# Optimization experiments

Measured on AMD Instinct MI355X. Metric: run time of the kernel, lower is better.

Reference implementation:

```python
import jax, jax.numpy as jnp
import numpy as np

N_T, N_C, N_D = 500_000, 200_000, 100_000  # target / card / device node counts
E = 1_000_000                              # edges per relation
IN, HID, OUT = 64, 64, 2


def setup_inputs() -> dict:
    key = jax.random.key(0)
    ks = jax.random.split(key, 18)
    f32 = jnp.float32
    inp = {
        "features": jax.random.normal(ks[0], (N_T, IN), f32),
        "emb_card": jax.random.normal(ks[1], (N_C, IN), f32) * 0.05,
        "emb_device": jax.random.normal(ks[2], (N_D, IN), f32) * 0.05,
        "W1": jax.random.normal(ks[3], (4, IN, HID), f32) * 0.05,
        "b1": jax.random.normal(ks[4], (4, HID), f32) * 0.05,
        "W2": jax.random.normal(ks[5], (4, HID, HID), f32) * 0.05,
        "b2": jax.random.normal(ks[6], (4, HID), f32) * 0.05,
        "W_out": jax.random.normal(ks[7], (HID, OUT), f32) * 0.05,
        "b_out": jax.random.normal(ks[8], (OUT,), f32) * 0.05,
        "src_c2t": jax.random.randint(ks[9], (E,), 0, N_C, jnp.int32),
        "dst_c2t": jax.random.randint(ks[10], (E,), 0, N_T, jnp.int32),
        "src_t2c": jax.random.randint(ks[11], (E,), 0, N_T, jnp.int32),
        "dst_t2c": jax.random.randint(ks[12], (E,), 0, N_C, jnp.int32),
        "src_d2t": jax.random.randint(ks[13], (E,), 0, N_D, jnp.int32),
        "dst_d2t": jax.random.randint(ks[14], (E,), 0, N_T, jnp.int32),
        "src_t2d": jax.random.randint(ks[15], (E,), 0, N_T, jnp.int32),
        "dst_t2d": jax.random.randint(ks[16], (E,), 0, N_D, jnp.int32),
    }
    return inp


def _mean_agg(Wh, src, dst, n_dst):
    """copy_u gather + scatter-mean: mean over incoming edges of Wh[src]."""
    msgs = Wh[src]  # [E, H] gather
    s = jax.ops.segment_sum(msgs, dst, num_segments=n_dst)
    deg = jax.ops.segment_sum(jnp.ones((src.shape[0],), Wh.dtype), dst, num_segments=n_dst)
    return s / jnp.maximum(deg, 1.0)[:, None]  # zero in-degree -> 0 (DGL default)


def _layer(x_t, x_c, x_d, W, b, edges):
    # etype order: 0 card->target, 1 target->card, 2 device->target, 3 target->device
    (sc2t, dc2t, st2c, dt2c, sd2t, dd2t, st2d, dt2d) = edges
    Wh0 = x_c @ W[0] + b[0]
    Wh1 = x_t @ W[1] + b[1]
    Wh2 = x_d @ W[2] + b[2]
    Wh3 = x_t @ W[3] + b[3]
    # cross-relation reducer = 'sum'
    h_t = _mean_agg(Wh0, sc2t, dc2t, N_T) + _mean_agg(Wh2, sd2t, dd2t, N_T)
    h_c = _mean_agg(Wh1, st2c, dt2c, N_C)
    h_d = _mean_agg(Wh3, st2d, dt2d, N_D)
    return h_t, h_c, h_d


def reference(features, emb_card, emb_device, W1, b1, W2, b2, W_out, b_out,
              src_c2t, dst_c2t, src_t2c, dst_t2c, src_d2t, dst_d2t, src_t2d, dst_t2d):
    edges = (src_c2t, dst_c2t, src_t2c, dst_t2c, src_d2t, dst_d2t, src_t2d, dst_t2d)
    h_t, h_c, h_d = _layer(features, emb_card, emb_device, W1, b1, edges)
    h_t, h_c, h_d = (jax.nn.leaky_relu(h, 0.01) for h in (h_t, h_c, h_d))
    h_t, h_c, h_d = _layer(h_t, h_c, h_d, W2, b2, edges)
    return h_t @ W_out + b_out  # [N_T, OUT] logits for target node type
```

## Files before the change

kernel.cpp:

```cpp
#include <hip/hip_runtime.h>
#include <hip/hip_bf16.h>


#define NT 500000
#define NC 200000
#define ND 100000
#define NE 1000000
#define H  64
#define CAP_T2C 32
#define CAP_T2D 48

#define PACK_SCALE 65536.0f
#define PACK_BIAS  262144
#define FIELD_MASK 0x3FFFFFFULL

#define NBK_MAX 245
#define OFF_C2T 196
#define OFF_D2T 441
#define EPB 4096
#define BPR 245
#define CAP_BK1 11776
#define CAP_BK2 4864

#define CB512 7813

__device__ __forceinline__ void rel_params(int rel, int& shift, int& hoff, int& nbk) {
    shift = (rel == 1) ? 10 : 11;
    hoff = (rel == 0) ? 0 : (rel == 1) ? 98 : (rel == 2) ? OFF_C2T : OFF_D2T;
    nbk = (rel < 2) ? 98 : 245;
}

__global__ __launch_bounds__(512)
void scatter_compress(const int* __restrict__ st2c, const int* __restrict__ dt2c,
                      const int* __restrict__ st2d, const int* __restrict__ dt2d,
                      const int* __restrict__ sc2t, const int* __restrict__ dc2t,
                      const int* __restrict__ sd2t, const int* __restrict__ dd2t,
                      int* __restrict__ cur,
                      unsigned long long* __restrict__ bedges1,
                      unsigned long long* __restrict__ bedges2,
                      const float* __restrict__ X, unsigned int* __restrict__ Xb,
                      const float* __restrict__ W2, const float* __restrict__ b2,
                      const float* __restrict__ Wout,
                      float* __restrict__ Wc, float* __restrict__ bc) {
    __shared__ unsigned long long le[EPB];
    __shared__ int h[NBK_MAX], pref[NBK_MAX], gbase[NBK_MAX], csr[NBK_MAX];
    __shared__ int sc[256];
    int t = threadIdx.x, b = blockIdx.x;

    if (b >= 4 * BPR) {
        int cb = b - 4 * BPR;
        if (cb < CB512) {
            size_t idx = (size_t)cb * 512 + t;
            if (idx < 4000000) {
                const float4 f0 = ((const float4*)X)[idx * 2];
                const float4 f1 = ((const float4*)X)[idx * 2 + 1];
                uint4 o;
                unsigned int u;
                #define BF(x) (u = __float_as_uint(x), (u + 0x7fffu + ((u >> 16) & 1u)) >> 16)
                o.x = BF(f0.x) | (BF(f0.y) << 16);
                o.y = BF(f0.z) | (BF(f0.w) << 16);
                o.z = BF(f1.x) | (BF(f1.y) << 16);
                o.w = BF(f1.z) | (BF(f1.w) << 16);
                #undef BF
                ((uint4*)Xb)[idx] = o;
            }
        } else if (t < 256) {
            int rel = t >> 7;
            int rem = t & 127;
            int k = rem >> 1, o = rem & 1;
            const float* W2r = W2 + (rel ? 2 : 0) * H * H;
            float s = 0.0f;
            for (int j = 0; j < H; ++j) s += W2r[k * H + j] * Wout[j * 2 + o];
            Wc[rel * 128 + k * 2 + o] = s;
            if (rem < 4) {
                int r2 = rem >> 1, o2 = rem & 1;
                const float* b2r = b2 + (r2 ? 2 : 0) * H;
                float sb = 0.0f;
                for (int j = 0; j < H; ++j) sb += b2r[j] * Wout[j * 2 + o2];
                bc[r2 * 2 + o2] = sb;
            }
        }
        return;
    }

    int rel = b / BPR;
    int bb = b - rel * BPR;
    const int* sp = (rel == 0) ? st2c : (rel == 1) ? st2d : (rel == 2) ? sc2t : sd2t;
    const int* dp = (rel == 0) ? dt2c : (rel == 1) ? dt2d : (rel == 2) ? dc2t : dd2t;
    int shift, hoff, nbk;
    rel_params(rel, shift, hoff, nbk);
    unsigned long long* bedges = (rel < 2) ? bedges1 : bedges2;
    int bkoff = (rel == 1) ? 98 : (rel == 3) ? 245 : 0;
    int bkcap = (rel < 2) ? CAP_BK1 : CAP_BK2;

    for (int i = t; i < nbk; i += 512) { h[i] = 0; csr[i] = 0; }
    __syncthreads();

    int base = bb * EPB + t * 8;
    bool ok = base < NE;
    int4 d0, d1, s0, s1;
    if (ok) {
        d0 = *(const int4*)(dp + base);
        d1 = *(const int4*)(dp + base + 4);
        s0 = *(const int4*)(sp + base);
        s1 = *(const int4*)(sp + base + 4);
        atomicAdd(&h[d0.x >> shift], 1);
        atomicAdd(&h[d0.y >> shift], 1);
        atomicAdd(&h[d0.z >> shift], 1);
        atomicAdd(&h[d0.w >> shift], 1);
        atomicAdd(&h[d1.x >> shift], 1);
        atomicAdd(&h[d1.y >> shift], 1);
        atomicAdd(&h[d1.z >> shift], 1);
        atomicAdd(&h[d1.w >> shift], 1);
    }
    __syncthreads();
    if (t < nbk && h[t]) gbase[t] = (bkoff + t) * bkcap + atomicAdd(&cur[hoff + t], h[t]);
    if (t < 256) sc[t] = (t < nbk) ? h[t] : 0;
    __syncthreads();
    for (int s = 1; s < 256; s <<= 1) {
        int y = (t < 256 && t >= s) ? sc[t - s] : 0;
        __syncthreads();
        if (t < 256) sc[t] += y;
        __syncthreads();
    }
    if (t < nbk) pref[t] = sc[t] - h[t];
    __syncthreads();

    if (ok) {
        #define BIN(dv, sv) { int k = (dv) >> shift; \
            int l = atomicAdd(&csr[k], 1); \
            le[pref[k] + l] = ((unsigned long long)(unsigned int)(dv) << 32) | (unsigned int)(sv); }
        BIN(d0.x, s0.x) BIN(d0.y, s0.y) BIN(d0.z, s0.z) BIN(d0.w, s0.w)
        BIN(d1.x, s1.x) BIN(d1.y, s1.y) BIN(d1.z, s1.z) BIN(d1.w, s1.w)
        #undef BIN
    }
    __syncthreads();

    int n_e = NE - bb * EPB; if (n_e > EPB) n_e = EPB;
    for (int i = t; i < n_e; i += 512) {
        unsigned long long e = le[i];
        int k = (int)(e >> 32) >> shift;
        bedges[(size_t)gbase[k] + (i - pref[k])] = e;
    }
}

__global__ __launch_bounds__(1024)
void radix_build(const unsigned long long* __restrict__ bedges1, const int* __restrict__ cur,
                 int* __restrict__ cnt_t2c, int* __restrict__ cols_t2c,
                 int* __restrict__ cnt_t2d, int* __restrict__ cols_t2d) {
    __shared__ int lc[2048];
    int t = threadIdx.x, k = blockIdx.x;
    int rel = k >= 98 ? 1 : 0;
    int shift = rel ? 10 : 11;
    int range = 1 << shift;
    int noff = (rel ? (k - 98) : k) << shift;
    int nN = rel ? ND : NC;
    int* cnt = rel ? cnt_t2d : cnt_t2c;
    int* cols = rel ? cols_t2d : cols_t2c;
    int cap = rel ? CAP_T2D : CAP_T2C;
    int e0 = k * CAP_BK1;
    int e1 = e0 + cur[k];
    for (int i = t; i < range; i += 1024) lc[i] = 0;
    __syncthreads();
    for (int i = e0 + t; i < e1; i += 1024) {
        unsigned long long e = bedges1[i];
        int d = (int)(e >> 32);
        int s = (int)(e & 0xffffffffu);
        int l = atomicAdd(&lc[d - noff], 1);
        if (l < cap) cols[(size_t)d * cap + l] = s;
    }
    __syncthreads();
    for (int i = t; i < range; i += 1024) {
        int gn = noff + i;
        if (gn < nN) cnt[gn] = lc[i];
    }
}

#define NBGM_C 3125
#define NBGM_D 1563

__global__ __launch_bounds__(512)
void gx_fused(const unsigned int* __restrict__ Xb,
              const int* __restrict__ cnt_c, const int* __restrict__ cols_c,
              const int* __restrict__ cnt_d, const int* __restrict__ cols_d,
              const float* __restrict__ W1, const float* __restrict__ b1,
              const float* __restrict__ Wc, const float* __restrict__ bc,
              float* __restrict__ Pc, float* __restrict__ Pd) {
    __shared__ float Xs[64][65];
    __shared__ float Wl[64][68];
    __shared__ float msk[64];
    int t = threadIdx.x;
    int lane = t & 63;
    int w = t >> 6;
    int half = lane >> 5;
    int li = lane & 31;

    int bn, nNodes, cap;
    const int* cnt; const int* cols;
    const float* W1r; const float* b1r; const float* Wcr; const float* bcr;
    float* P;
    if (blockIdx.x < NBGM_C) {
        bn = blockIdx.x * 64; nNodes = NC; cap = CAP_T2C;
        cnt = cnt_c; cols = cols_c;
        W1r = W1 + 1 * H * H; b1r = b1 + 1 * H; Wcr = Wc; bcr = bc; P = Pc;
    } else {
        bn = (blockIdx.x - NBGM_C) * 64; nNodes = ND; cap = CAP_T2D;
        cnt = cnt_d; cols = cols_d;
        W1r = W1 + 3 * H * H; b1r = b1 + 3 * H; Wcr = Wc + 128; bcr = bc + 2; P = Pd;
    }

    for (int q = t; q < 1024; q += 512) {
        int kk = q >> 4, s2 = q & 15;
        *(float4*)&Wl[kk][s2 * 4] = *(const float4*)(W1r + kk * H + s2 * 4);
    }

    int gnb = bn + w * 8;
    int cval = 0;
    if (lane < 8 && gnb + lane < nNodes) cval = cnt[gnb + lane];

    int cc[8], mm[8], cv[8];
#pragma unroll
    for (int r = 0; r < 8; ++r) {
        cc[r] = __shfl(cval, r);
        mm[r] = cc[r] < cap ? cc[r] : cap;
    }
#pragma unroll
    for (int r = 0; r < 8; ++r) {
        int gn = gnb + r;
        cv[r] = (lane < mm[r] && gn < nNodes) ? cols[(size_t)gn * cap + lane] : 0;
    }

    int maxm = 0;
#pragma unroll
    for (int r = 0; r < 8; ++r) maxm = maxm > mm[r] ? maxm : mm[r];

    float ax[8], ay[8];
#pragma unroll
    for (int r = 0; r < 8; ++r) { ax[r] = 0.0f; ay[r] = 0.0f; }

    for (int j = 0; j < maxm; j += 2) {
#pragma unroll
        for (int r = 0; r < 8; ++r) {
            int sA = __shfl(cv[r], j);
            int sB = __shfl(cv[r], j + 1);
            int src = half ? sB : sA;
            unsigned int v = 0;
            if (j + half < mm[r]) v = Xb[(size_t)src * 32 + li];
            ax[r] += __uint_as_float(v << 16);
            ay[r] += __uint_as_float(v & 0xffff0000u);
        }
    }

#pragma unroll
    for (int r = 0; r < 8; ++r) {
        float fx = ax[r] + __shfl_xor(ax[r], 32);
        float fy = ay[r] + __shfl_xor(ay[r], 32);
        float inv = cc[r] > 0 ? 1.0f / (float)cc[r] : 0.0f;
        ax[r] = fx * inv; ay[r] = fy * inv;
    }
#pragma unroll
    for (int r = 0; r < 8; r += 2) {
        int nl = w * 8 + r + half;
        float2 v = half ? make_float2(ax[r + 1], ay[r + 1]) : make_float2(ax[r], ay[r]);
        *(float2*)&Xs[nl][li * 2] = v;
    }
    if (lane < 8) msk[w * 8 + lane] = (cval > 0) ? 1.0f : 0.0f;
    __syncthreads();

    int nl = t >> 3;
    int c0 = (t & 7) * 8;
    float4 ba = *(const float4*)(b1r + c0);
    float4 bb4 = *(const float4*)(b1r + c0 + 4);
    float h0 = ba.x, h1 = ba.y, h2 = ba.z, h3 = ba.w;
    float h4 = bb4.x, h5 = bb4.y, h6 = bb4.z, h7 = bb4.w;
#pragma unroll
    for (int k = 0; k < H; ++k) {
        float xv = Xs[nl][k];
        float4 wa = *(const float4*)&Wl[k][c0];
        float4 wb = *(const float4*)&Wl[k][c0 + 4];
        h0 = fmaf(xv, wa.x, h0); h1 = fmaf(xv, wa.y, h1);
        h2 = fmaf(xv, wa.z, h2); h3 = fmaf(xv, wa.w, h3);
        h4 = fmaf(xv, wb.x, h4); h5 = fmaf(xv, wb.y, h5);
        h6 = fmaf(xv, wb.z, h6); h7 = fmaf(xv, wb.w, h7);
    }
    float m = msk[nl];
    h0 = (h0 > 0.f ? h0 : 0.01f * h0) * m;
    h1 = (h1 > 0.f ? h1 : 0.01f * h1) * m;
    h2 = (h2 > 0.f ? h2 : 0.01f * h2) * m;
    h3 = (h3 > 0.f ? h3 : 0.01f * h3) * m;
    h4 = (h4 > 0.f ? h4 : 0.01f * h4) * m;
    h5 = (h5 > 0.f ? h5 : 0.01f * h5) * m;
    h6 = (h6 > 0.f ? h6 : 0.01f * h6) * m;
    h7 = (h7 > 0.f ? h7 : 0.01f * h7) * m;
    float4 wc0 = *(const float4*)(Wcr + c0 * 2);
    float4 wc1 = *(const float4*)(Wcr + c0 * 2 + 4);
    float4 wc2 = *(const float4*)(Wcr + c0 * 2 + 8);
    float4 wc3 = *(const float4*)(Wcr + c0 * 2 + 12);
    float p0 = h0 * wc0.x + h1 * wc0.z + h2 * wc1.x + h3 * wc1.z
             + h4 * wc2.x + h5 * wc2.z + h6 * wc3.x + h7 * wc3.z;
    float p1 = h0 * wc0.y + h1 * wc0.w + h2 * wc1.y + h3 * wc1.w
             + h4 * wc2.y + h5 * wc2.w + h6 * wc3.y + h7 * wc3.w;
#pragma unroll
    for (int off = 1; off < 8; off <<= 1) {
        p0 += __shfl_xor(p0, off);
        p1 += __shfl_xor(p1, off);
    }
    int gn = bn + nl;
    if ((t & 7) == 0 && gn < nNodes) {
        float2 o = make_float2(p0 + bcr[0], p1 + bcr[1]);
        *(float2*)(P + 2 * (size_t)gn) = o;
    }
}

__device__ __forceinline__ unsigned long long pack_p(const float* __restrict__ P, int s) {
    float2 pv = *(const float2*)(P + 2 * (size_t)s);
    float a = fminf(fmaxf(pv.x, -3.99f), 3.99f);
    float b = fminf(fmaxf(pv.y, -3.99f), 3.99f);
    unsigned int ia = (unsigned int)(__float2int_rn(a * PACK_SCALE) + PACK_BIAS);
    unsigned int ib = (unsigned int)(__float2int_rn(b * PACK_SCALE) + PACK_BIAS);
    return (1ULL << 52) | ((unsigned long long)ia << 26) | (unsigned long long)ib;
}

__global__ __launch_bounds__(1024)
void agg_out(const unsigned long long* __restrict__ bedges2, const int* __restrict__ cur,
             const float* __restrict__ Pc, const float* __restrict__ Pd,
             const float* __restrict__ bout, float* __restrict__ out) {
    __shared__ unsigned long long accC[2048], accD[2048];
    int t = threadIdx.x, k = blockIdx.x;
    int noff = k << 11;
    int range = NT - noff; if (range > 2048) range = 2048;
    for (int i = t; i < 2048; i += 1024) { accC[i] = 0ULL; accD[i] = 0ULL; }
    __syncthreads();

    int e0 = k * CAP_BK2, e1 = e0 + cur[OFF_C2T + k];
    for (int i = e0 + t; i < e1; i += 1024) {
        unsigned long long e = bedges2[i];
        int d = (int)(e >> 32);
        int s = (int)(e & 0xffffffffu);
        atomicAdd(&accC[d - noff], pack_p(Pc, s));
    }
    int f0 = (245 + k) * CAP_BK2, f1 = f0 + cur[OFF_D2T + k];
    for (int i = f0 + t; i < f1; i += 1024) {
        unsigned long long e = bedges2[i];
        int d = (int)(e >> 32);
        int s = (int)(e & 0xffffffffu);
        atomicAdd(&accD[d - noff], pack_p(Pd, s));
    }
    __syncthreads();

    float bo0 = bout[0], bo1 = bout[1];
    const float inv_s = 1.0f / PACK_SCALE;
    for (int i = t; i < range; i += 1024) {
        unsigned long long xc = accC[i];
        unsigned long long xd = accD[i];
        int dc = (int)(xc >> 52);
        int dd = (int)(xd >> 52);
        float ic = dc > 0 ? 1.0f / (float)dc : 0.0f;
        float id = dd > 0 ? 1.0f / (float)dd : 0.0f;
        float c0 = (float)((long long)((xc >> 26) & FIELD_MASK) - (long long)dc * PACK_BIAS);
        float c1 = (float)((long long)(xc & FIELD_MASK) - (long long)dc * PACK_BIAS);
        float d0 = (float)((long long)((xd >> 26) & FIELD_MASK) - (long long)dd * PACK_BIAS);
        float d1 = (float)((long long)(xd & FIELD_MASK) - (long long)dd * PACK_BIAS);
        float2 o;
        o.x = bo0 + (c0 * ic + d0 * id) * inv_s;
        o.y = bo1 + (c1 * ic + d1 * id) * inv_s;
        *(float2*)(out + 2 * (size_t)(noff + i)) = o;
    }
}

extern "C" void kernel_launch(void* const* d_in, const int* in_sizes, int n_in,
                              void* d_out, int out_size, void* d_ws, size_t ws_size,
                              hipStream_t stream) {
    const float* features = (const float*)d_in[0];
    const float* W1 = (const float*)d_in[3];
    const float* b1 = (const float*)d_in[4];
    const float* W2 = (const float*)d_in[5];
    const float* b2 = (const float*)d_in[6];
    const float* W_out = (const float*)d_in[7];
    const float* b_out = (const float*)d_in[8];
    const int* src_c2t = (const int*)d_in[9];
    const int* dst_c2t = (const int*)d_in[10];
    const int* src_t2c = (const int*)d_in[11];
    const int* dst_t2c = (const int*)d_in[12];
    const int* src_d2t = (const int*)d_in[13];
    const int* dst_d2t = (const int*)d_in[14];
    const int* src_t2d = (const int*)d_in[15];
    const int* dst_t2d = (const int*)d_in[16];
    float* out = (float*)d_out;

    char* w = (char*)d_ws;
    int* cur = (int*)w;                           w += 1024 * 4;
    size_t zero_bytes = 1024 * 4;
    int* cnt_t2c = (int*)w;                       w += (size_t)NC * 4;
    int* cnt_t2d = (int*)w;                       w += (size_t)ND * 4;
    int* cols_t2c = (int*)w;                      w += (size_t)NC * CAP_T2C * 4;
    int* cols_t2d = (int*)w;                      w += (size_t)ND * CAP_T2D * 4;
    float* p_c = (float*)w;                       w += (size_t)NC * 2 * 4;
    float* p_d = (float*)w;                       w += (size_t)ND * 2 * 4;
    float* Wc = (float*)w;                        w += 256 * 4;
    float* bc = (float*)w;                        w += 16;
    unsigned long long* bedges1 = (unsigned long long*)w;  w += (size_t)196 * CAP_BK1 * 8;
    unsigned long long* bedges2 = (unsigned long long*)w;  w += (size_t)490 * CAP_BK2 * 8;
    unsigned int* Xb = (unsigned int*)w;          w += (size_t)NT * H * 2;

    hipMemsetAsync(d_ws, 0, zero_bytes, stream);

    scatter_compress<<<4 * BPR + CB512 + 1, 512, 0, stream>>>(
        src_t2c, dst_t2c, src_t2d, dst_t2d,
        src_c2t, dst_c2t, src_d2t, dst_d2t,
        cur, bedges1, bedges2,
        features, Xb, W2, b2, W_out, Wc, bc);

    radix_build<<<196, 1024, 0, stream>>>(bedges1, cur,
                                          cnt_t2c, cols_t2c, cnt_t2d, cols_t2d);

    gx_fused<<<NBGM_C + NBGM_D, 512, 0, stream>>>(
        Xb, cnt_t2c, cols_t2c, cnt_t2d, cols_t2d,
        W1, b1, Wc, bc, p_c, p_d);

    agg_out<<<NBK_MAX, 1024, 0, stream>>>(bedges2, cur, p_c, p_d, b_out, out);
}
```

Measured before the change: 210.4 us.

## Split fused gather-mean and 64x64 transform into two kernels via bf16 buffer

Splits the fused gather-plus-matmul kernel in two. The first kernel does the neighbor mean gather and writes bf16-packed means to a new workspace buffer. The second loads those rows into shared memory and does the W1/Wc projection. This frees the gather kernel from the large shared-memory tiles and the W1 load, which may raise occupancy and latency hiding for the irregular gathers. In exchange it adds a launch, an extra global round trip of about 38 MB, and one more bf16 rounding of the mean.

```diff
diff --git a/kernel.cpp b/kernel.cpp
--- a/kernel.cpp
+++ b/kernel.cpp
@@ -29,6 +29,8 @@
     hoff = (rel == 0) ? 0 : (rel == 1) ? 98 : (rel == 2) ? OFF_C2T : OFF_D2T;
     nbk = (rel < 2) ? 98 : 245;
 }
+
+#define BFP(x) (u = __float_as_uint(x), (u + 0x7fffu + ((u >> 16) & 1u)) >> 16)
 
 __global__ __launch_bounds__(512)
 void scatter_compress(const int* __restrict__ st2c, const int* __restrict__ dt2c,
@@ -56,12 +58,10 @@
                 const float4 f1 = ((const float4*)X)[idx * 2 + 1];
                 uint4 o;
                 unsigned int u;
-                #define BF(x) (u = __float_as_uint(x), (u + 0x7fffu + ((u >> 16) & 1u)) >> 16)
-                o.x = BF(f0.x) | (BF(f0.y) << 16);
-                o.y = BF(f0.z) | (BF(f0.w) << 16);
-                o.z = BF(f1.x) | (BF(f1.y) << 16);
-                o.w = BF(f1.z) | (BF(f1.w) << 16);
-                #undef BF
+                o.x = BFP(f0.x) | (BFP(f0.y) << 16);
+                o.y = BFP(f0.z) | (BFP(f0.w) << 16);
+                o.z = BFP(f1.x) | (BFP(f1.y) << 16);
+                o.w = BFP(f1.z) | (BFP(f1.w) << 16);
                 ((uint4*)Xb)[idx] = o;
             }
         } else if (t < 256) {
@@ -180,15 +180,10 @@
 #define NBGM_D 1563
 
 __global__ __launch_bounds__(512)
-void gx_fused(const unsigned int* __restrict__ Xb,
-              const int* __restrict__ cnt_c, const int* __restrict__ cols_c,
-              const int* __restrict__ cnt_d, const int* __restrict__ cols_d,
-              const float* __restrict__ W1, const float* __restrict__ b1,
-              const float* __restrict__ Wc, const float* __restrict__ bc,
-              float* __restrict__ Pc, float* __restrict__ Pd) {
-    __shared__ float Xs[64][65];
-    __shared__ float Wl[64][68];
-    __shared__ float msk[64];
+void gather_mean(const unsigned int* __restrict__ Xb,
+                 const int* __restrict__ cnt_c, const int* __restrict__ cols_c,
+                 const int* __restrict__ cnt_d, const int* __restrict__ cols_d,
+                 unsigned int* __restrict__ mB) {
     int t = threadIdx.x;
     int lane = t & 63;
     int w = t >> 6;
@@ -196,22 +191,13 @@
     int li = lane & 31;
 
     int bn, nNodes, cap;
-    const int* cnt; const int* cols;
-    const float* W1r; const float* b1r; const float* Wcr; const float* bcr;
-    float* P;
+    const int* cnt; const int* cols; unsigned int* mP;
     if (blockIdx.x < NBGM_C) {
         bn = blockIdx.x * 64; nNodes = NC; cap = CAP_T2C;
-        cnt = cnt_c; cols = cols_c;
-        W1r = W1 + 1 * H * H; b1r = b1 + 1 * H; Wcr = Wc; bcr = bc; P = Pc;
+        cnt = cnt_c; cols = cols_c; mP = mB;
     } else {
         bn = (blockIdx.x - NBGM_C) * 64; nNodes = ND; cap = CAP_T2D;
-        cnt = cnt_d; cols = cols_d;
-        W1r = W1 + 3 * H * H; b1r = b1 + 3 * H; Wcr = Wc + 128; bcr = bc + 2; P = Pd;
-    }
-
-    for (int q = t; q < 1024; q += 512) {
-        int kk = q >> 4, s2 = q & 15;
-        *(float4*)&Wl[kk][s2 * 4] = *(const float4*)(W1r + kk * H + s2 * 4);
+        cnt = cnt_d; cols = cols_d; mP = mB + (size_t)NC * 32;
     }
 
     int gnb = bn + w * 8;
@@ -258,13 +244,60 @@
         float inv = cc[r] > 0 ? 1.0f / (float)cc[r] : 0.0f;
         ax[r] = fx * inv; ay[r] = fy * inv;
     }
+    unsigned int u;
 #pragma unroll
     for (int r = 0; r < 8; r += 2) {
-        int nl = w * 8 + r + half;
-        float2 v = half ? make_float2(ax[r + 1], ay[r + 1]) : make_float2(ax[r], ay[r]);
-        *(float2*)&Xs[nl][li * 2] = v;
-    }
-    if (lane < 8) msk[w * 8 + lane] = (cval > 0) ? 1.0f : 0.0f;
+        int gn = gnb + r + half;
+        float vx = half ? ax[r + 1] : ax[r];
+        float vy = half ? ay[r + 1] : ay[r];
+        unsigned int pv = BFP(vx) | (BFP(vy) << 16);
+        if (gn < nNodes) mP[(size_t)gn * 32 + li] = pv;
+    }
+}
+
+#define NBX_C 3125
+#define NBX_D 1563
+
+__global__ __launch_bounds__(512)
+void xform64(const unsigned int* __restrict__ mB,
+             const int* __restrict__ cnt_c, const int* __restrict__ cnt_d,
+             const float* __restrict__ W1, const float* __restrict__ b1,
+             const float* __restrict__ Wc, const float* __restrict__ bc,
+             float* __restrict__ Pc, float* __restrict__ Pd) {
+    __shared__ float Xs[64][65];
+    __shared__ float Wl[64][68];
+    __shared__ float msk[64];
+    int t = threadIdx.x;
+
+    int bn, nNodes; const unsigned int* mrow; const int* cnt;
+    const float* W1r; const float* b1r; const float* Wcr; const float* bcr;
+    float* P;
+    if (blockIdx.x < NBX_C) {
+        bn = blockIdx.x * 64; nNodes = NC;
+        mrow = mB; cnt = cnt_c;
+        W1r = W1 + 1 * H * H; b1r = b1 + 1 * H; Wcr = Wc; bcr = bc; P = Pc;
+    } else {
+        bn = (blockIdx.x - NBX_C) * 64; nNodes = ND;
+        mrow = mB + (size_t)NC * 32; cnt = cnt_d;
+        W1r = W1 + 3 * H * H; b1r = b1 + 3 * H; Wcr = Wc + 128; bcr = bc + 2; P = Pd;
+    }
+
+    {
+        int nl = t >> 3, seg = t & 7;
+        int gn = bn + nl;
+        uint4 v = make_uint4(0, 0, 0, 0);
+        if (gn < nNodes) v = ((const uint4*)(mrow + (size_t)gn * 32))[seg];
+        float* xr = &Xs[nl][seg * 8];
+        xr[0] = __uint_as_float(v.x << 16); xr[1] = __uint_as_float(v.x & 0xffff0000u);
+        xr[2] = __uint_as_float(v.y << 16); xr[3] = __uint_as_float(v.y & 0xffff0000u);
+        xr[4] = __uint_as_float(v.z << 16); xr[5] = __uint_as_float(v.z & 0xffff0000u);
+        xr[6] = __uint_as_float(v.w << 16); xr[7] = __uint_as_float(v.w & 0xffff0000u);
+        for (int q = t; q < 1024; q += 512) {
+            int kk = q >> 4, s2 = q & 15;
+            *(float4*)&Wl[kk][s2 * 4] = *(const float4*)(W1r + kk * H + s2 * 4);
+        }
+        if (t < 64) msk[t] = (bn + t < nNodes && cnt[bn + t] > 0) ? 1.0f : 0.0f;
+    }
     __syncthreads();
 
     int nl = t >> 3;
@@ -402,6 +435,7 @@
     unsigned long long* bedges1 = (unsigned long long*)w;  w += (size_t)196 * CAP_BK1 * 8;
     unsigned long long* bedges2 = (unsigned long long*)w;  w += (size_t)490 * CAP_BK2 * 8;
     unsigned int* Xb = (unsigned int*)w;          w += (size_t)NT * H * 2;
+    unsigned int* mB = (unsigned int*)w;          w += ((size_t)(NC + ND) + 64) * 32 * 4;
 
     hipMemsetAsync(d_ws, 0, zero_bytes, stream);
 
@@ -414,9 +448,11 @@
     radix_build<<<196, 1024, 0, stream>>>(bedges1, cur,
                                           cnt_t2c, cols_t2c, cnt_t2d, cols_t2d);
 
-    gx_fused<<<NBGM_C + NBGM_D, 512, 0, stream>>>(
-        Xb, cnt_t2c, cols_t2c, cnt_t2d, cols_t2d,
-        W1, b1, Wc, bc, p_c, p_d);
+    gather_mean<<<NBGM_C + NBGM_D, 512, 0, stream>>>(
+        Xb, cnt_t2c, cols_t2c, cnt_t2d, cols_t2d, mB);
+
+    xform64<<<NBX_C + NBX_D, 512, 0, stream>>>(
+        mB, cnt_t2c, cnt_t2d, W1, b1, Wc, bc, p_c, p_d);
 
     agg_out<<<NBK_MAX, 1024, 0, stream>>>(bedges2, cur, p_c, p_d, b_out, out);
 }
```

Result: slower. 240.6 us (+14.3%).
